# Kernel tuning notes

Hardware: AMD Instinct MI355X
Metric: run time of the kernel (lower is better)

## Reference

```python
import jax, jax.numpy as jnp
from jax import lax
import numpy as np

NPOINTS = 1024
B, N, C = 32, 100000, 3


def setup_inputs() -> dict:
    key = jax.random.key(0)
    k1, k2 = jax.random.split(key)
    coord = jax.random.normal(k1, (B, N, C), dtype=jnp.float32)
    farthest_init = jax.random.randint(k2, (B,), 0, N, dtype=jnp.int64)
    return {"coord": coord, "farthest_init": farthest_init}


def reference(coord, farthest_init):
    # coord: (B, N, 3); farthest_init: (B,) seed indices.
    Bs, Ns, _ = coord.shape
    init_distance = jnp.full((Bs, Ns), 1e10, dtype=coord.dtype)

    def step(carry, _):
        distance, farthest = carry
        # gather current centroid per batch: (B, 1, 3)
        centroid = jnp.take_along_axis(coord, farthest[:, None, None], axis=1)
        dist = jnp.sum((coord - centroid) ** 2, axis=-1)  # (B, N)
        distance = jnp.minimum(distance, dist)            # masked update
        new_farthest = jnp.argmax(distance, axis=-1)      # (B,)
        # record the index that was just used as centroid (pre-update), as in torch loop
        return (distance, new_farthest), farthest

    (_, _), centroids_t = lax.scan(step, (init_distance, farthest_init), None, length=NPOINTS)
    centroids = centroids_t.T  # (B, NPOINTS)
    # gather sampled coordinates: (B, NPOINTS, 3)
    sampled = jnp.take_along_axis(coord, centroids[:, :, None], axis=1)
    return centroids, sampled
```

## Files before the change

### kernel.cpp

```cpp
#include <hip/hip_runtime.h>
#include <stdint.h>

#define BATCHES 32
#define NPT     100000
#define NSAMP   1024
#define GPB     16
#define NPAIR   16
#define TPB     1024
#define NCW     15
#define CTH     (NCW*64)
#define PPB     6250
#define PPT     7
#define TAILT   490

typedef unsigned long long u64;
typedef unsigned int u32;

#define WS_BYTES (2 * BATCHES * GPB * 4 * 8)

__device__ __forceinline__ void red_ki(u64& key, u32& idx, int off) {
    u64 ok = __shfl_xor(key, off, 64);
    u32 oi = __shfl_xor(idx, off, 64);
    if (ok > key || (ok == key && oi < idx)) { key = ok; idx = oi; }
}

__device__ __forceinline__ void red_step(u64& key, u32& idx, float& x, float& y, float& z, int off) {
    u64   ok = __shfl_xor(key, off, 64);
    u32   oi = __shfl_xor(idx, off, 64);
    float ox = __shfl_xor(x, off, 64);
    float oy = __shfl_xor(y, off, 64);
    float oz = __shfl_xor(z, off, 64);
    if (ok > key || (ok == key && oi < idx)) { key = ok; idx = oi; x = ox; y = oy; z = oz; }
}

__global__ void
__attribute__((amdgpu_flat_work_group_size(TPB, TPB), amdgpu_waves_per_eu(4, 4)))
fps_kernel(const float* __restrict__ coord,
           const int* __restrict__ seed_raw,
           float* __restrict__ out,
           u64* __restrict__ rec)
{
    const int tid  = threadIdx.x;
    const int lane = tid & 63;
    const int wid  = tid >> 6;
    const int p    = (int)blockIdx.x & (NPAIR - 1);
    const int g    = (int)blockIdx.x >> 4;
    const int base = g * PPB;
    const int bA = p, bB = p + NPAIR;

    __shared__ u64 winw[2][2][2];
    __shared__ u32 sbar[8];
    __shared__ u64   pkey[2][NCW];
    __shared__ u32   pidx[2][NCW];
    __shared__ float pxs[2][NCW], pys[2][NCW], pzs[2][NCW];

    if (tid < 8) { sbar[tid] = 0; ((u64*)winw)[tid] = 0ull; }
    __syncthreads();

    float* cent_out = out;
    float* samp_out = out + BATCHES * NSAMP;

    if (wid == NCW) {
        for (int t = 1; t < NSAMP; ++t) {
            #pragma unroll
            for (int xb = 0; xb < 2; ++xb) {
                const int batch = xb ? bB : bA;
                u64* slot = rec + ((size_t)((t & 1) * BATCHES + batch) * GPB) * 4;
                const u64 t2 = (u64)(((t >> 1) + 1) & 3);
                const bool mine = lane < 3 * GPB;
                u64* wp = slot + (mine ? ((lane / 3) * 4 + (lane % 3)) : 0);
                u64 w = 0;
                for (;;) {
                    bool ok = true;
                    if (mine) {
                        w = __hip_atomic_load(wp, __ATOMIC_RELAXED, __HIP_MEMORY_SCOPE_AGENT);
                        ok = (w >> 62) == t2;
                    }
                    if (__ballot(ok) == ~0ull) break;
                    __builtin_amdgcn_s_sleep(1);
                }
                const int li = lane & 15;
                u64 w0 = __shfl(w, 3 * li + 0, 64);
                u64 w1 = __shfl(w, 3 * li + 1, 64);
                u64 w2 = __shfl(w, 3 * li + 2, 64);
                u64 k3 = 0ull; u32 i3 = 0xFFFFFFFFu; float x3 = 0.f, y3 = 0.f, z3 = 0.f;
                if (lane < GPB) {
                    k3 = (w0 & 0x3FFFFFFFFFFFFFFFull) | (((w1 >> 60) & 3ull) << 62);
                    u32 xbt = (u32)(w1 >> 28);
                    u32 ybt = (u32)(((w1 & 0xFFFFFFFull) << 4) | ((w2 >> 58) & 0xFull));
                    u32 zbt = (u32)(w2 >> 26);
                    i3 = (u32)((w2 >> 9) & 0x1FFFFu);
                    x3 = __uint_as_float(xbt); y3 = __uint_as_float(ybt); z3 = __uint_as_float(zbt);
                }
                red_step(k3, i3, x3, y3, z3, 8); red_step(k3, i3, x3, y3, z3, 4);
                red_step(k3, i3, x3, y3, z3, 2); red_step(k3, i3, x3, y3, z3, 1);
                if (lane == 0) {
                    u32 xbt = __float_as_uint(x3), ybt = __float_as_uint(y3), zbt = __float_as_uint(z3);
                    u64 v0 = (t2 << 62) | ((u64)xbt << 30) | (u64)(ybt >> 2);
                    u64 v1 = (t2 << 62) | ((u64)(ybt & 3u) << 60) | ((u64)zbt << 28) | ((u64)i3 << 11);
                    __hip_atomic_store(&winw[xb][t & 1][0], v0, __ATOMIC_RELAXED, __HIP_MEMORY_SCOPE_WORKGROUP);
                    __hip_atomic_store(&winw[xb][t & 1][1], v1, __ATOMIC_RELAXED, __HIP_MEMORY_SCOPE_WORKGROUP);
                }
            }
        }
        return;
    }

    const int ct = tid;
    const float* cbA = coord + (size_t)bA * (NPT * 3);
    const float* cbB = coord + (size_t)bB * (NPT * 3);

    int odd = 0;
    #pragma unroll
    for (int i = 1; i < 32; i += 2) odd |= seed_raw[i];
    u32 scur[2]; float scx[2], scy[2], scz[2];
    scur[0] = (u32)((odd == 0) ? seed_raw[2 * bA] : seed_raw[bA]);
    scur[1] = (u32)((odd == 0) ? seed_raw[2 * bB] : seed_raw[bB]);
    scx[0] = cbA[(size_t)scur[0] * 3 + 0]; scy[0] = cbA[(size_t)scur[0] * 3 + 1]; scz[0] = cbA[(size_t)scur[0] * 3 + 2];
    scx[1] = cbB[(size_t)scur[1] * 3 + 0]; scy[1] = cbB[(size_t)scur[1] * 3 + 1]; scz[1] = cbB[(size_t)scur[1] * 3 + 2];

    float  px[2][PPT], py[2][PPT], pz[2][PPT];
    double d[2][PPT];
    #pragma unroll
    for (int xb = 0; xb < 2; ++xb) {
        const float* cb = xb ? cbB : cbA;
        #pragma unroll
        for (int k = 0; k < PPT; ++k) {
            bool v = (k < PPT - 1) || (ct < TAILT);
            int gi = base + (v ? (k * CTH + ct) : 0);
            px[xb][k] = v ? cb[(size_t)gi * 3 + 0] : 0.f;
            py[xb][k] = v ? cb[(size_t)gi * 3 + 1] : 0.f;
            pz[xb][k] = v ? cb[(size_t)gi * 3 + 2] : 0.f;
            d[xb][k]  = v ? 1.0e10 : 0.0;
        }
    }

    for (int t = 0; t < NSAMP; ++t) {
        #pragma unroll
        for (int xb = 0; xb < 2; ++xb) {
            const int batch = xb ? bB : bA;
            const int pi = 2 * t + xb;
            u32 cur; float cx, cy, cz;
            if (t == 0) {
                cur = scur[xb]; cx = scx[xb]; cy = scy[xb]; cz = scz[xb];
            } else {
                const u64 t2 = (u64)(((t >> 1) + 1) & 3);
                u64 v0, v1;
                for (;;) {
                    v0 = __hip_atomic_load(&winw[xb][t & 1][0], __ATOMIC_RELAXED, __HIP_MEMORY_SCOPE_WORKGROUP);
                    v1 = __hip_atomic_load(&winw[xb][t & 1][1], __ATOMIC_RELAXED, __HIP_MEMORY_SCOPE_WORKGROUP);
                    if (((v0 >> 62) == t2) & ((v1 >> 62) == t2)) break;
                }
                u32 xbt = (u32)(v0 >> 30);
                u32 ybt = (u32)(((v0 & 0x3FFFFFFFull) << 2) | ((v1 >> 60) & 3ull));
                u32 zbt = (u32)(v1 >> 28);
                cur = (u32)((v1 >> 11) & 0x1FFFFu);
                cx = __uint_as_float(xbt); cy = __uint_as_float(ybt); cz = __uint_as_float(zbt);
            }
            if (g == 0 && wid == 1 && lane == 0) {
                cent_out[batch * NSAMP + t] = (float)cur;
                size_t so = ((size_t)batch * NSAMP + t) * 3;
                samp_out[so + 0] = cx; samp_out[so + 1] = cy; samp_out[so + 2] = cz;
            }
            if (t == NSAMP - 1) continue;

            const double cxd = (double)cx, cyd = (double)cy, czd = (double)cz;
            double bd = -1.0; u32 bi = 0; float bx = 0.f, by = 0.f, bz = 0.f;
            #pragma unroll
            for (int k = 0; k < PPT; ++k) {
                if (k == PPT - 1 && ct >= TAILT) break;
                double dx = __dsub_rn((double)px[xb][k], cxd);
                double dy = __dsub_rn((double)py[xb][k], cyd);
                double dz = __dsub_rn((double)pz[xb][k], czd);
                double d2 = __dadd_rn(__dadd_rn(__dmul_rn(dx, dx), __dmul_rn(dy, dy)),
                                      __dmul_rn(dz, dz));
                double nd = fmin(d[xb][k], d2);
                d[xb][k] = nd;
                bool gt = nd > bd;
                bd = gt ? nd : bd;
                bi = gt ? (u32)(base + k * CTH + ct) : bi;
                bx = gt ? px[xb][k] : bx;
                by = gt ? py[xb][k] : by;
                bz = gt ? pz[xb][k] : bz;
            }
            u64 key = (u64)__double_as_longlong(bd);

            u64 wk = key; u32 wi = bi;
            red_ki(wk, wi, 32); red_ki(wk, wi, 16); red_ki(wk, wi, 8);
            red_ki(wk, wi, 4);  red_ki(wk, wi, 2);  red_ki(wk, wi, 1);
            const int pb = pi & 1;
            if (wi == bi) { pkey[pb][wid] = wk; pidx[pb][wid] = wi;
                            pxs[pb][wid] = bx; pys[pb][wid] = by; pzs[pb][wid] = bz; }

            if (lane == 0)
                __hip_atomic_fetch_add(&sbar[pi & 7], 1u, __ATOMIC_RELEASE, __HIP_MEMORY_SCOPE_WORKGROUP);
            const u32 tgt = (u32)(NCW * ((pi >> 3) + 1));
            while (__hip_atomic_load(&sbar[pi & 7], __ATOMIC_ACQUIRE, __HIP_MEMORY_SCOPE_WORKGROUP) < tgt) {}

            if (wid == 0) {
                u64   k2 = (lane < NCW) ? pkey[pb][lane] : 0ull;
                u32   i2 = (lane < NCW) ? pidx[pb][lane] : 0xFFFFFFFFu;
                float x2 = (lane < NCW) ? pxs[pb][lane] : 0.f;
                float y2 = (lane < NCW) ? pys[pb][lane] : 0.f;
                float z2 = (lane < NCW) ? pzs[pb][lane] : 0.f;
                red_step(k2, i2, x2, y2, z2, 8); red_step(k2, i2, x2, y2, z2, 4);
                red_step(k2, i2, x2, y2, z2, 2); red_step(k2, i2, x2, y2, z2, 1);
                if (lane == 0) {
                    const u32 v = (u32)(t + 1);
                    const u64 t2p = (u64)(((v >> 1) + 1) & 3);
                    u64* r = rec + ((size_t)((v & 1) * BATCHES + batch) * GPB + g) * 4;
                    u32 xbt = __float_as_uint(x2), ybt = __float_as_uint(y2), zbt = __float_as_uint(z2);
                    u64 w0 = (t2p << 62) | (k2 & 0x3FFFFFFFFFFFFFFFull);
                    u64 w1 = (t2p << 62) | ((k2 >> 62) << 60) | ((u64)xbt << 28) | (u64)(ybt >> 4);
                    u64 w2 = (t2p << 62) | ((u64)(ybt & 0xFu) << 58) | ((u64)zbt << 26) | ((u64)i2 << 9);
                    __hip_atomic_store(&r[0], w0, __ATOMIC_RELAXED, __HIP_MEMORY_SCOPE_AGENT);
                    __hip_atomic_store(&r[1], w1, __ATOMIC_RELAXED, __HIP_MEMORY_SCOPE_AGENT);
                    __hip_atomic_store(&r[2], w2, __ATOMIC_RELAXED, __HIP_MEMORY_SCOPE_AGENT);
                }
            }
        }
    }
}

extern "C" void kernel_launch(void* const* d_in, const int* in_sizes, int n_in,
                              void* d_out, int out_size, void* d_ws, size_t ws_size,
                              hipStream_t stream)
{
    const float* coord = (const float*)d_in[0];
    const int*   seed  = (const int*)d_in[1];
    float* out = (float*)d_out;
    u64* rec = (u64*)d_ws;

    hipMemsetAsync(d_ws, 0, WS_BYTES, stream);
    fps_kernel<<<dim3(NPAIR * GPB), dim3(TPB), 0, stream>>>(coord, seed, out, rec);
}
```

Measured before the change: 4.373 ms.

## Assign one batch per block with 8 blocks per batch instead of paired batches

Restructures the work split: each block now handles a single batch over 12500 points (14 per thread) with 8 cooperating blocks per batch, instead of two interleaved batches over 6250 points across 16 blocks. The grid stays at 256 blocks, but each block runs one dependency chain per step instead of two, and the cross-block merge reduces over 8 records instead of 16. The cost is that the two independent batches no longer overlap to hide each other's synchronisation latency, and there are twice as many points per thread in registers.

```diff
diff --git a/kernel.cpp b/kernel.cpp
--- a/kernel.cpp
+++ b/kernel.cpp
@@ -4,14 +4,13 @@
 #define BATCHES 32
 #define NPT     100000
 #define NSAMP   1024
-#define GPB     16
-#define NPAIR   16
+#define GPB     8
 #define TPB     1024
 #define NCW     15
 #define CTH     (NCW*64)
-#define PPB     6250
-#define PPT     7
-#define TAILT   490
+#define PPB     12500
+#define PPT     14
+#define TAILT   20
 
 typedef unsigned long long u64;
 typedef unsigned int u32;
@@ -43,180 +42,166 @@
     const int tid  = threadIdx.x;
     const int lane = tid & 63;
     const int wid  = tid >> 6;
-    const int p    = (int)blockIdx.x & (NPAIR - 1);
-    const int g    = (int)blockIdx.x >> 4;
+    const int b    = (int)blockIdx.x & (BATCHES - 1);
+    const int g    = (int)blockIdx.x >> 5;
     const int base = g * PPB;
-    const int bA = p, bB = p + NPAIR;
-
-    __shared__ u64 winw[2][2][2];
+
+    __shared__ u64 winw[2][2];
     __shared__ u32 sbar[8];
     __shared__ u64   pkey[2][NCW];
     __shared__ u32   pidx[2][NCW];
     __shared__ float pxs[2][NCW], pys[2][NCW], pzs[2][NCW];
 
-    if (tid < 8) { sbar[tid] = 0; ((u64*)winw)[tid] = 0ull; }
+    if (tid < 8) sbar[tid] = 0;
+    if (tid < 4) ((u64*)winw)[tid] = 0ull;
     __syncthreads();
 
     float* cent_out = out;
     float* samp_out = out + BATCHES * NSAMP;
 
     if (wid == NCW) {
+        const bool mine = lane < 3 * GPB;
+        const int  widx = mine ? ((lane / 3) * 4 + (lane % 3)) : 0;
         for (int t = 1; t < NSAMP; ++t) {
-            #pragma unroll
-            for (int xb = 0; xb < 2; ++xb) {
-                const int batch = xb ? bB : bA;
-                u64* slot = rec + ((size_t)((t & 1) * BATCHES + batch) * GPB) * 4;
-                const u64 t2 = (u64)(((t >> 1) + 1) & 3);
-                const bool mine = lane < 3 * GPB;
-                u64* wp = slot + (mine ? ((lane / 3) * 4 + (lane % 3)) : 0);
-                u64 w = 0;
-                for (;;) {
-                    bool ok = true;
-                    if (mine) {
-                        w = __hip_atomic_load(wp, __ATOMIC_RELAXED, __HIP_MEMORY_SCOPE_AGENT);
-                        ok = (w >> 62) == t2;
-                    }
-                    if (__ballot(ok) == ~0ull) break;
-                    __builtin_amdgcn_s_sleep(1);
+            u64* slot = rec + ((size_t)((t & 1) * BATCHES + b) * GPB) * 4;
+            u64* wp   = slot + widx;
+            const u64 t2 = (u64)(((t >> 1) + 1) & 3);
+            u64 w = 0;
+            for (;;) {
+                bool ok = true;
+                if (mine) {
+                    w = __hip_atomic_load(wp, __ATOMIC_RELAXED, __HIP_MEMORY_SCOPE_AGENT);
+                    ok = (w >> 62) == t2;
                 }
-                const int li = lane & 15;
-                u64 w0 = __shfl(w, 3 * li + 0, 64);
-                u64 w1 = __shfl(w, 3 * li + 1, 64);
-                u64 w2 = __shfl(w, 3 * li + 2, 64);
-                u64 k3 = 0ull; u32 i3 = 0xFFFFFFFFu; float x3 = 0.f, y3 = 0.f, z3 = 0.f;
-                if (lane < GPB) {
-                    k3 = (w0 & 0x3FFFFFFFFFFFFFFFull) | (((w1 >> 60) & 3ull) << 62);
-                    u32 xbt = (u32)(w1 >> 28);
-                    u32 ybt = (u32)(((w1 & 0xFFFFFFFull) << 4) | ((w2 >> 58) & 0xFull));
-                    u32 zbt = (u32)(w2 >> 26);
-                    i3 = (u32)((w2 >> 9) & 0x1FFFFu);
-                    x3 = __uint_as_float(xbt); y3 = __uint_as_float(ybt); z3 = __uint_as_float(zbt);
-                }
-                red_step(k3, i3, x3, y3, z3, 8); red_step(k3, i3, x3, y3, z3, 4);
-                red_step(k3, i3, x3, y3, z3, 2); red_step(k3, i3, x3, y3, z3, 1);
-                if (lane == 0) {
-                    u32 xbt = __float_as_uint(x3), ybt = __float_as_uint(y3), zbt = __float_as_uint(z3);
-                    u64 v0 = (t2 << 62) | ((u64)xbt << 30) | (u64)(ybt >> 2);
-                    u64 v1 = (t2 << 62) | ((u64)(ybt & 3u) << 60) | ((u64)zbt << 28) | ((u64)i3 << 11);
-                    __hip_atomic_store(&winw[xb][t & 1][0], v0, __ATOMIC_RELAXED, __HIP_MEMORY_SCOPE_WORKGROUP);
-                    __hip_atomic_store(&winw[xb][t & 1][1], v1, __ATOMIC_RELAXED, __HIP_MEMORY_SCOPE_WORKGROUP);
-                }
+                if (__ballot(ok) == ~0ull) break;
+                __builtin_amdgcn_s_sleep(1);
+            }
+            const int li = lane & 7;
+            u64 w0 = __shfl(w, 3 * li + 0, 64);
+            u64 w1 = __shfl(w, 3 * li + 1, 64);
+            u64 w2 = __shfl(w, 3 * li + 2, 64);
+            u64 k3 = 0ull; u32 i3 = 0xFFFFFFFFu; float x3 = 0.f, y3 = 0.f, z3 = 0.f;
+            if (lane < GPB) {
+                k3 = (w0 & 0x3FFFFFFFFFFFFFFFull) | (((w1 >> 60) & 3ull) << 62);
+                u32 xbt = (u32)(w1 >> 28);
+                u32 ybt = (u32)(((w1 & 0xFFFFFFFull) << 4) | ((w2 >> 58) & 0xFull));
+                u32 zbt = (u32)(w2 >> 26);
+                i3 = (u32)((w2 >> 9) & 0x1FFFFu);
+                x3 = __uint_as_float(xbt); y3 = __uint_as_float(ybt); z3 = __uint_as_float(zbt);
+            }
+            red_step(k3, i3, x3, y3, z3, 4); red_step(k3, i3, x3, y3, z3, 2);
+            red_step(k3, i3, x3, y3, z3, 1);
+            if (lane == 0) {
+                u32 xbt = __float_as_uint(x3), ybt = __float_as_uint(y3), zbt = __float_as_uint(z3);
+                u64 v0 = (t2 << 62) | ((u64)xbt << 30) | (u64)(ybt >> 2);
+                u64 v1 = (t2 << 62) | ((u64)(ybt & 3u) << 60) | ((u64)zbt << 28) | ((u64)i3 << 11);
+                __hip_atomic_store(&winw[t & 1][0], v0, __ATOMIC_RELAXED, __HIP_MEMORY_SCOPE_WORKGROUP);
+                __hip_atomic_store(&winw[t & 1][1], v1, __ATOMIC_RELAXED, __HIP_MEMORY_SCOPE_WORKGROUP);
             }
         }
         return;
     }
 
     const int ct = tid;
-    const float* cbA = coord + (size_t)bA * (NPT * 3);
-    const float* cbB = coord + (size_t)bB * (NPT * 3);
+    const float* cb = coord + (size_t)b * (NPT * 3);
 
     int odd = 0;
     #pragma unroll
     for (int i = 1; i < 32; i += 2) odd |= seed_raw[i];
-    u32 scur[2]; float scx[2], scy[2], scz[2];
-    scur[0] = (u32)((odd == 0) ? seed_raw[2 * bA] : seed_raw[bA]);
-    scur[1] = (u32)((odd == 0) ? seed_raw[2 * bB] : seed_raw[bB]);
-    scx[0] = cbA[(size_t)scur[0] * 3 + 0]; scy[0] = cbA[(size_t)scur[0] * 3 + 1]; scz[0] = cbA[(size_t)scur[0] * 3 + 2];
-    scx[1] = cbB[(size_t)scur[1] * 3 + 0]; scy[1] = cbB[(size_t)scur[1] * 3 + 1]; scz[1] = cbB[(size_t)scur[1] * 3 + 2];
-
-    float  px[2][PPT], py[2][PPT], pz[2][PPT];
-    double d[2][PPT];
+    u32 scur = (u32)((odd == 0) ? seed_raw[2 * b] : seed_raw[b]);
+    float scx = cb[(size_t)scur * 3 + 0];
+    float scy = cb[(size_t)scur * 3 + 1];
+    float scz = cb[(size_t)scur * 3 + 2];
+
+    float  px[PPT], py[PPT], pz[PPT];
+    double d[PPT];
     #pragma unroll
-    for (int xb = 0; xb < 2; ++xb) {
-        const float* cb = xb ? cbB : cbA;
+    for (int k = 0; k < PPT; ++k) {
+        bool v = (k < PPT - 1) || (ct < TAILT);
+        int gi = base + (v ? (k * CTH + ct) : 0);
+        px[k] = v ? cb[(size_t)gi * 3 + 0] : 0.f;
+        py[k] = v ? cb[(size_t)gi * 3 + 1] : 0.f;
+        pz[k] = v ? cb[(size_t)gi * 3 + 2] : 0.f;
+        d[k]  = v ? 1.0e10 : 0.0;
+    }
+
+    for (int t = 0; t < NSAMP; ++t) {
+        u32 cur; float cx, cy, cz;
+        if (t == 0) {
+            cur = scur; cx = scx; cy = scy; cz = scz;
+        } else {
+            const u64 t2 = (u64)(((t >> 1) + 1) & 3);
+            u64 v0, v1;
+            for (;;) {
+                v0 = __hip_atomic_load(&winw[t & 1][0], __ATOMIC_RELAXED, __HIP_MEMORY_SCOPE_WORKGROUP);
+                v1 = __hip_atomic_load(&winw[t & 1][1], __ATOMIC_RELAXED, __HIP_MEMORY_SCOPE_WORKGROUP);
+                if (((v0 >> 62) == t2) & ((v1 >> 62) == t2)) break;
+            }
+            u32 xbt = (u32)(v0 >> 30);
+            u32 ybt = (u32)(((v0 & 0x3FFFFFFFull) << 2) | ((v1 >> 60) & 3ull));
+            u32 zbt = (u32)(v1 >> 28);
+            cur = (u32)((v1 >> 11) & 0x1FFFFu);
+            cx = __uint_as_float(xbt); cy = __uint_as_float(ybt); cz = __uint_as_float(zbt);
+        }
+        if (g == 0 && wid == 1 && lane == 0) {
+            cent_out[b * NSAMP + t] = (float)cur;
+            size_t so = ((size_t)b * NSAMP + t) * 3;
+            samp_out[so + 0] = cx; samp_out[so + 1] = cy; samp_out[so + 2] = cz;
+        }
+        if (t == NSAMP - 1) continue;
+
+        const double cxd = (double)cx, cyd = (double)cy, czd = (double)cz;
+        double bd = -1.0; u32 bi = 0; float bx = 0.f, by = 0.f, bz = 0.f;
         #pragma unroll
         for (int k = 0; k < PPT; ++k) {
-            bool v = (k < PPT - 1) || (ct < TAILT);
-            int gi = base + (v ? (k * CTH + ct) : 0);
-            px[xb][k] = v ? cb[(size_t)gi * 3 + 0] : 0.f;
-            py[xb][k] = v ? cb[(size_t)gi * 3 + 1] : 0.f;
-            pz[xb][k] = v ? cb[(size_t)gi * 3 + 2] : 0.f;
-            d[xb][k]  = v ? 1.0e10 : 0.0;
-        }
-    }
-
-    for (int t = 0; t < NSAMP; ++t) {
-        #pragma unroll
-        for (int xb = 0; xb < 2; ++xb) {
-            const int batch = xb ? bB : bA;
-            const int pi = 2 * t + xb;
-            u32 cur; float cx, cy, cz;
-            if (t == 0) {
-                cur = scur[xb]; cx = scx[xb]; cy = scy[xb]; cz = scz[xb];
-            } else {
-                const u64 t2 = (u64)(((t >> 1) + 1) & 3);
-                u64 v0, v1;
-                for (;;) {
-                    v0 = __hip_atomic_load(&winw[xb][t & 1][0], __ATOMIC_RELAXED, __HIP_MEMORY_SCOPE_WORKGROUP);
-                    v1 = __hip_atomic_load(&winw[xb][t & 1][1], __ATOMIC_RELAXED, __HIP_MEMORY_SCOPE_WORKGROUP);
-                    if (((v0 >> 62) == t2) & ((v1 >> 62) == t2)) break;
-                }
-                u32 xbt = (u32)(v0 >> 30);
-                u32 ybt = (u32)(((v0 & 0x3FFFFFFFull) << 2) | ((v1 >> 60) & 3ull));
-                u32 zbt = (u32)(v1 >> 28);
-                cur = (u32)((v1 >> 11) & 0x1FFFFu);
-                cx = __uint_as_float(xbt); cy = __uint_as_float(ybt); cz = __uint_as_float(zbt);
-            }
-            if (g == 0 && wid == 1 && lane == 0) {
-                cent_out[batch * NSAMP + t] = (float)cur;
-                size_t so = ((size_t)batch * NSAMP + t) * 3;
-                samp_out[so + 0] = cx; samp_out[so + 1] = cy; samp_out[so + 2] = cz;
-            }
-            if (t == NSAMP - 1) continue;
-
-            const double cxd = (double)cx, cyd = (double)cy, czd = (double)cz;
-            double bd = -1.0; u32 bi = 0; float bx = 0.f, by = 0.f, bz = 0.f;
-            #pragma unroll
-            for (int k = 0; k < PPT; ++k) {
-                if (k == PPT - 1 && ct >= TAILT) break;
-                double dx = __dsub_rn((double)px[xb][k], cxd);
-                double dy = __dsub_rn((double)py[xb][k], cyd);
-                double dz = __dsub_rn((double)pz[xb][k], czd);
-                double d2 = __dadd_rn(__dadd_rn(__dmul_rn(dx, dx), __dmul_rn(dy, dy)),
-                                      __dmul_rn(dz, dz));
-                double nd = fmin(d[xb][k], d2);
-                d[xb][k] = nd;
-                bool gt = nd > bd;
-                bd = gt ? nd : bd;
-                bi = gt ? (u32)(base + k * CTH + ct) : bi;
-                bx = gt ? px[xb][k] : bx;
-                by = gt ? py[xb][k] : by;
-                bz = gt ? pz[xb][k] : bz;
-            }
-            u64 key = (u64)__double_as_longlong(bd);
-
-            u64 wk = key; u32 wi = bi;
-            red_ki(wk, wi, 32); red_ki(wk, wi, 16); red_ki(wk, wi, 8);
-            red_ki(wk, wi, 4);  red_ki(wk, wi, 2);  red_ki(wk, wi, 1);
-            const int pb = pi & 1;
-            if (wi == bi) { pkey[pb][wid] = wk; pidx[pb][wid] = wi;
-                            pxs[pb][wid] = bx; pys[pb][wid] = by; pzs[pb][wid] = bz; }
-
-            if (lane == 0)
-                __hip_atomic_fetch_add(&sbar[pi & 7], 1u, __ATOMIC_RELEASE, __HIP_MEMORY_SCOPE_WORKGROUP);
-            const u32 tgt = (u32)(NCW * ((pi >> 3) + 1));
-            while (__hip_atomic_load(&sbar[pi & 7], __ATOMIC_ACQUIRE, __HIP_MEMORY_SCOPE_WORKGROUP) < tgt) {}
-
-            if (wid == 0) {
-                u64   k2 = (lane < NCW) ? pkey[pb][lane] : 0ull;
-                u32   i2 = (lane < NCW) ? pidx[pb][lane] : 0xFFFFFFFFu;
-                float x2 = (lane < NCW) ? pxs[pb][lane] : 0.f;
-                float y2 = (lane < NCW) ? pys[pb][lane] : 0.f;
-                float z2 = (lane < NCW) ? pzs[pb][lane] : 0.f;
-                red_step(k2, i2, x2, y2, z2, 8); red_step(k2, i2, x2, y2, z2, 4);
-                red_step(k2, i2, x2, y2, z2, 2); red_step(k2, i2, x2, y2, z2, 1);
-                if (lane == 0) {
-                    const u32 v = (u32)(t + 1);
-                    const u64 t2p = (u64)(((v >> 1) + 1) & 3);
-                    u64* r = rec + ((size_t)((v & 1) * BATCHES + batch) * GPB + g) * 4;
-                    u32 xbt = __float_as_uint(x2), ybt = __float_as_uint(y2), zbt = __float_as_uint(z2);
-                    u64 w0 = (t2p << 62) | (k2 & 0x3FFFFFFFFFFFFFFFull);
-                    u64 w1 = (t2p << 62) | ((k2 >> 62) << 60) | ((u64)xbt << 28) | (u64)(ybt >> 4);
-                    u64 w2 = (t2p << 62) | ((u64)(ybt & 0xFu) << 58) | ((u64)zbt << 26) | ((u64)i2 << 9);
-                    __hip_atomic_store(&r[0], w0, __ATOMIC_RELAXED, __HIP_MEMORY_SCOPE_AGENT);
-                    __hip_atomic_store(&r[1], w1, __ATOMIC_RELAXED, __HIP_MEMORY_SCOPE_AGENT);
-                    __hip_atomic_store(&r[2], w2, __ATOMIC_RELAXED, __HIP_MEMORY_SCOPE_AGENT);
-                }
+            if (k == PPT - 1 && ct >= TAILT) break;
+            double dx = __dsub_rn((double)px[k], cxd);
+            double dy = __dsub_rn((double)py[k], cyd);
+            double dz = __dsub_rn((double)pz[k], czd);
+            double d2 = __dadd_rn(__dadd_rn(__dmul_rn(dx, dx), __dmul_rn(dy, dy)),
+                                  __dmul_rn(dz, dz));
+            double nd = fmin(d[k], d2);
+            d[k] = nd;
+            bool gt = nd > bd;
+            bd = gt ? nd : bd;
+            bi = gt ? (u32)(base + k * CTH + ct) : bi;
+            bx = gt ? px[k] : bx;
+            by = gt ? py[k] : by;
+            bz = gt ? pz[k] : bz;
+        }
+        u64 key = (u64)__double_as_longlong(bd);
+
+        u64 wk = key; u32 wi = bi;
+        red_ki(wk, wi, 32); red_ki(wk, wi, 16); red_ki(wk, wi, 8);
+        red_ki(wk, wi, 4);  red_ki(wk, wi, 2);  red_ki(wk, wi, 1);
+        const int pb = t & 1;
+        if (wi == bi) { pkey[pb][wid] = wk; pidx[pb][wid] = wi;
+                        pxs[pb][wid] = bx; pys[pb][wid] = by; pzs[pb][wid] = bz; }
+
+        if (lane == 0)
+            __hip_atomic_fetch_add(&sbar[t & 7], 1u, __ATOMIC_RELEASE, __HIP_MEMORY_SCOPE_WORKGROUP);
+        const u32 tgt = (u32)(NCW * ((t >> 3) + 1));
+        while (__hip_atomic_load(&sbar[t & 7], __ATOMIC_ACQUIRE, __HIP_MEMORY_SCOPE_WORKGROUP) < tgt) {}
+
+        if (wid == 0) {
+            u64   k2 = (lane < NCW) ? pkey[pb][lane] : 0ull;
+            u32   i2 = (lane < NCW) ? pidx[pb][lane] : 0xFFFFFFFFu;
+            float x2 = (lane < NCW) ? pxs[pb][lane] : 0.f;
+            float y2 = (lane < NCW) ? pys[pb][lane] : 0.f;
+            float z2 = (lane < NCW) ? pzs[pb][lane] : 0.f;
+            red_step(k2, i2, x2, y2, z2, 8); red_step(k2, i2, x2, y2, z2, 4);
+            red_step(k2, i2, x2, y2, z2, 2); red_step(k2, i2, x2, y2, z2, 1);
+            if (lane == 0) {
+                const u32 v = (u32)(t + 1);
+                const u64 t2p = (u64)(((v >> 1) + 1) & 3);
+                u64* r = rec + ((size_t)((v & 1) * BATCHES + b) * GPB + g) * 4;
+                u32 xbt = __float_as_uint(x2), ybt = __float_as_uint(y2), zbt = __float_as_uint(z2);
+                u64 w0 = (t2p << 62) | (k2 & 0x3FFFFFFFFFFFFFFFull);
+                u64 w1 = (t2p << 62) | ((k2 >> 62) << 60) | ((u64)xbt << 28) | (u64)(ybt >> 4);
+                u64 w2 = (t2p << 62) | ((u64)(ybt & 0xFu) << 58) | ((u64)zbt << 26) | ((u64)i2 << 9);
+                __hip_atomic_store(&r[0], w0, __ATOMIC_RELAXED, __HIP_MEMORY_SCOPE_AGENT);
+                __hip_atomic_store(&r[1], w1, __ATOMIC_RELAXED, __HIP_MEMORY_SCOPE_AGENT);
+                __hip_atomic_store(&r[2], w2, __ATOMIC_RELAXED, __HIP_MEMORY_SCOPE_AGENT);
             }
         }
     }
@@ -232,5 +217,5 @@
     u64* rec = (u64*)d_ws;
 
     hipMemsetAsync(d_ws, 0, WS_BYTES, stream);
-    fps_kernel<<<dim3(NPAIR * GPB), dim3(TPB), 0, stream>>>(coord, seed, out, rec);
-}
+    fps_kernel<<<dim3(BATCHES * GPB), dim3(TPB), 0, stream>>>(coord, seed, out, rec);
+}
```

Result: slower. 5.245 ms (+20.0%).
